# Optimization experiments

Hardware: AMD Instinct MI355X
Metric: run time of the kernel (lower is better)

The kernel has to match this reference:

```python
import jax, jax.numpy as jnp
import numpy as np

HEAD_DIM = 256
V_DIM = 256
HIDDEN = 1024
SCALE_BASE = 512
GAMMA = 0.96875
BATCH, SEQ = 4, 4096


def _dup_interleave(m):
    # (L, d/2) -> (L, d), duplicating each column consecutively
    return jnp.repeat(m, 2, axis=-1)


def _rotate_every_two(x):
    x1 = x[..., ::2]
    x2 = x[..., 1::2]
    return jnp.stack([-x2, x1], axis=-1).reshape(x.shape)


def _xpos(x, downscale=False):
    # x: (B, L, head_dim); offset=0 path of XPOS.forward
    B, L, Dh = x.shape
    half = Dh // 2
    scale_buf = (jnp.arange(0, Dh, 2, dtype=jnp.float32) + 0.4 * Dh) / (1.4 * Dh)  # (half,)
    pos = jnpp = jnp.arange(L, dtype=jnp.float32)
    scale = scale_buf[None, :] ** (pos / SCALE_BASE)[:, None]  # (L, half)
    inv_freq = 1.0 / (10000.0 ** (jnp.arange(half, dtype=jnp.float32) / half))
    sinusoid = pos[:, None] * inv_freq[None, :]  # (L, half)
    sin, cos = jnp.sin(sinusoid), jnp.cos(sinusoid)
    if downscale:
        scale = 1.0 / scale
    cos_s = _dup_interleave(cos * scale)  # (L, Dh)
    sin_s = _dup_interleave(sin * scale)
    return x * cos_s[None] + _rotate_every_two(x) * sin_s[None]


def _decay_matrix(L):
    n = jnp.arange(L)[:, None]
    m = jnp.arange(L)[None, :]
    mask = n >= m
    expo = jnp.where(mask, n - m, 0).astype(jnp.float32)
    return jnp.where(mask, GAMMA ** expo, 0.0)  # (L, L)


def setup_inputs() -> dict:
    key = jax.random.key(0)
    k1, k2, k3, k4 = jax.random.split(key, 4)
    X = jax.random.normal(k1, (BATCH, SEQ, HIDDEN), dtype=jnp.float32)
    W_Q = jax.random.normal(k2, (HIDDEN, HEAD_DIM), dtype=jnp.float32) / HIDDEN
    W_K = jax.random.normal(k3, (HIDDEN, HEAD_DIM), dtype=jnp.float32) / HIDDEN
    W_V = jax.random.normal(k4, (HIDDEN, V_DIM), dtype=jnp.float32) / HIDDEN
    return {"X": X, "W_Q": W_Q, "W_K": W_K, "W_V": W_V}


def reference(X, W_Q, W_K, W_V):
    L = X.shape[1]
    Q = _xpos(X @ W_Q)                      # (B, L, Dh)
    K = _xpos(X @ W_K, downscale=True)      # (B, L, Dh)
    V = X @ W_V                             # (B, L, Dv)
    D = _decay_matrix(L)                    # (L, L)
    ret = jnp.einsum('bqd,bkd->bqk', Q, K) * D[None]  # (B, L, L)
    return ret @ V                          # (B, L, Dv)
```

## Files before the change

### kernel.cpp

```cpp
#include <hip/hip_runtime.h>
#include <hip/hip_bf16.h>
#include <cstdint>
#include <cstddef>

#define L_SEQ 4096
#define BATCH_N 4
#define HID 1024
#define DH 256
#define LOG2_GAMMA (-0.045803689613124953f)

typedef __attribute__((ext_vector_type(8))) short short8;
typedef __attribute__((ext_vector_type(4))) float floatx4;

__device__ __forceinline__ unsigned short f2bf(float f) {
    union { float f; unsigned int u; } v; v.f = f;
    unsigned int r = (v.u + 0x7FFFu + ((v.u >> 16) & 1u)) >> 16;
    return (unsigned short)r;
}

__device__ __forceinline__ void async_copy16(const unsigned short* gsrc,
                                             unsigned short* lds) {
    __builtin_amdgcn_global_load_lds(
        (const __attribute__((address_space(1))) unsigned int*)gsrc,
        (__attribute__((address_space(3))) unsigned int*)lds, 16, 0, 0);
}

__global__ __launch_bounds__(256) void convert_x_kernel(
    const float* __restrict__ X, unsigned short* __restrict__ Xb)
{
    const int i = (blockIdx.x * 256 + threadIdx.x) * 4;
    const float4 v = *(const float4*)&X[i];
    ushort4 p;
    p.x = f2bf(v.x); p.y = f2bf(v.y); p.z = f2bf(v.z); p.w = f2bf(v.w);
    *(ushort4*)&Xb[i] = p;
}

__global__ __launch_bounds__(256) void transpose_w_kernel(
    const float* __restrict__ WQ, const float* __restrict__ WK,
    const float* __restrict__ WV, unsigned short* __restrict__ Wt)
{
    __shared__ float Ts[64][68];
    const int n0 = blockIdx.x * 64;
    const int k0 = blockIdx.y * 64;
    const int seg = n0 >> 8;
    const float* __restrict__ W = (seg == 0) ? WQ : (seg == 1) ? WK : WV;
    const int nl0 = n0 & 255;

    const int t  = threadIdx.x;
    const int r  = t >> 4;
    const int c4 = (t & 15) * 4;
    #pragma unroll
    for (int i = 0; i < 4; ++i) {
        const int kk = r + i * 16;
        const float4 v = *(const float4*)&W[(size_t)(k0 + kk) * DH + nl0 + c4];
        Ts[c4 + 0][kk] = v.x;
        Ts[c4 + 1][kk] = v.y;
        Ts[c4 + 2][kk] = v.z;
        Ts[c4 + 3][kk] = v.w;
    }
    __syncthreads();
    const int rn = t >> 3;
    const int c8 = (t & 7) * 8;
    #pragma unroll
    for (int i = 0; i < 2; ++i) {
        const int rr = rn + i * 32;
        ushort4 p0, p1;
        p0.x = f2bf(Ts[rr][c8 + 0]); p0.y = f2bf(Ts[rr][c8 + 1]);
        p0.z = f2bf(Ts[rr][c8 + 2]); p0.w = f2bf(Ts[rr][c8 + 3]);
        p1.x = f2bf(Ts[rr][c8 + 4]); p1.y = f2bf(Ts[rr][c8 + 5]);
        p1.z = f2bf(Ts[rr][c8 + 6]); p1.w = f2bf(Ts[rr][c8 + 7]);
        unsigned short* dst = &Wt[(size_t)(n0 + rr) * HID + k0 + c8];
        *(ushort4*)dst       = p0;
        *(ushort4*)(dst + 4) = p1;
    }
}

__global__ __launch_bounds__(256) void gemm_qkv_kernel(
    const unsigned short* __restrict__ Wt,
    const unsigned short* __restrict__ Xb,
    unsigned short* __restrict__ Qo,
    unsigned short* __restrict__ Ko,
    unsigned short* __restrict__ VtG)
{
    __shared__ unsigned short Wa[128][32];
    __shared__ unsigned short Xs[128][32];

    const int n0 = blockIdx.x * 128;
    const int p0 = blockIdx.y * 128;
    const int t    = threadIdx.x;
    const int w    = t >> 6;
    const int lane = t & 63;
    const int quad = lane >> 4;
    const int l16  = lane & 15;
    const int wn   = (w & 1) * 64;
    const int wp   = (w >> 1) * 64;

    const int srow = w * 32 + (lane >> 2);
    const int scol = (lane & 3) * 8;

    floatx4 acc[4][4];
    #pragma unroll
    for (int i = 0; i < 4; ++i)
        #pragma unroll
        for (int j = 0; j < 4; ++j) acc[i][j] = (floatx4){0.f, 0.f, 0.f, 0.f};

    for (int k0 = 0; k0 < HID; k0 += 32) {
        __syncthreads();
        #pragma unroll
        for (int is = 0; is < 2; ++is) {
            const unsigned short* ga =
                &Wt[(size_t)(n0 + srow + is * 16) * HID + k0 + scol];
            const unsigned short* gb =
                &Xb[(size_t)(p0 + srow + is * 16) * HID + k0 + scol];
            async_copy16(ga, &Wa[w * 32 + is * 16][0]);
            async_copy16(gb, &Xs[w * 32 + is * 16][0]);
        }
        __syncthreads();

        short8 af[4], bf[4];
        #pragma unroll
        for (int nt = 0; nt < 4; ++nt)
            af[nt] = *(const short8*)&Wa[wn + nt * 16 + l16][quad * 8];
        #pragma unroll
        for (int pt = 0; pt < 4; ++pt)
            bf[pt] = *(const short8*)&Xs[wp + pt * 16 + l16][quad * 8];
        #pragma unroll
        for (int nt = 0; nt < 4; ++nt)
            #pragma unroll
            for (int pt = 0; pt < 4; ++pt)
                acc[nt][pt] = __builtin_amdgcn_mfma_f32_16x16x32_bf16(
                    af[nt], bf[pt], acc[nt][pt], 0, 0, 0);
    }

    const int seg = n0 >> 8;
    #pragma unroll
    for (int nt = 0; nt < 4; ++nt) {
        const int nfeat = n0 + wn + nt * 16 + quad * 4;
        const int d0 = nfeat & 255;
        #pragma unroll
        for (int pt = 0; pt < 4; ++pt) {
            const int pg  = p0 + wp + pt * 16 + l16;
            const int b   = pg >> 12;
            const int pos = pg & (L_SEQ - 1);
            if (seg == 2) {
                #pragma unroll
                for (int g = 0; g < 4; ++g)
                    VtG[(((size_t)(b * 256 + d0 + g)) << 12) + pos] =
                        f2bf(acc[nt][pt][g]);
            } else {
                const float e = (float)pos * (1.0f / 512.0f);
                float res[4];
                #pragma unroll
                for (int h = 0; h < 4; h += 2) {
                    const int d  = d0 + h;
                    const int i2 = d >> 1;
                    const float sb = ((float)d + 102.4f) * (1.0f / 358.4f);
                    float sc = exp2f(log2f(sb) * e);
                    if (seg == 1) sc = 1.0f / sc;
                    const float invf = exp2f(-13.287712379549449f *
                                             ((float)i2 * (1.0f / 128.0f)));
                    float s, c;
                    sincosf((float)pos * invf, &s, &c);
                    const float cs = c * sc, ss = s * sc;
                    const float xe = acc[nt][pt][h], xo = acc[nt][pt][h + 1];
                    res[h]     = xe * cs - xo * ss;
                    res[h + 1] = xo * cs + xe * ss;
                }
                ushort4 pk;
                pk.x = f2bf(res[0]); pk.y = f2bf(res[1]);
                pk.z = f2bf(res[2]); pk.w = f2bf(res[3]);
                unsigned short* orow =
                    ((seg == 0) ? Qo : Ko) + (size_t)pg * DH + d0;
                *(ushort4*)orow = pk;
            }
        }
    }
}

__global__ __launch_bounds__(256) void retention_kernel(
    const unsigned short* __restrict__ Q,
    const unsigned short* __restrict__ K,
    const unsigned short* __restrict__ VtG,
    float* __restrict__ O)
{
    __shared__ short Qs[64][264];
    __shared__ short Ks[32][264];
    __shared__ short Vt[256][40];
    __shared__ short Ss[64][40];

    const int qt = blockIdx.x;
    const int b  = blockIdx.y;
    const int t  = threadIdx.x;
    const int q0 = qt * 64;

    const int w    = t >> 6;
    const int lane = t & 63;
    const int quad = lane >> 4;
    const int l16  = lane & 15;
    const int w16  = w * 16;

    const size_t rbase = (size_t)b * L_SEQ * DH;
    const size_t vbase = ((size_t)b * DH) << 12;

    {
        const unsigned short* src = Q + rbase + (size_t)q0 * DH;
        #pragma unroll
        for (int i = 0; i < 8; ++i) {
            const int row = i * 8 + (t >> 5);
            const int col = (t & 31) * 8;
            *(uint4*)&Qs[row][col] = *(const uint4*)&src[row * DH + col];
        }
    }

    floatx4 o[16];
    #pragma unroll
    for (int f = 0; f < 16; ++f) o[f] = (floatx4){0.f, 0.f, 0.f, 0.f};

    int kstart = q0 - 512;
    if (kstart < 0) kstart = 0;

    for (int k0 = kstart; k0 < q0 + 64; k0 += 32) {
        __syncthreads();
        {
            const unsigned short* src = K + rbase + (size_t)k0 * DH;
            #pragma unroll
            for (int i = 0; i < 4; ++i) {
                const int row = i * 8 + (t >> 5);
                const int col = (t & 31) * 8;
                *(uint4*)&Ks[row][col] = *(const uint4*)&src[row * DH + col];
            }
        }
        {
            const int koff = (t & 7) * 4;
            #pragma unroll
            for (int i = 0; i < 8; ++i) {
                const int c = (t >> 3) + 32 * i;
                *(uint2*)&Vt[c][koff] =
                    *(const uint2*)&VtG[vbase + ((size_t)c << 12) + k0 + koff];
            }
        }
        __syncthreads();

        #pragma unroll
        for (int ntile = 0; ntile < 2; ++ntile) {
            floatx4 s = (floatx4){0.f, 0.f, 0.f, 0.f};
            #pragma unroll
            for (int d8 = 0; d8 < 8; ++d8) {
                const short8 a   = *(const short8*)&Qs[w16 + l16][d8 * 32 + quad * 8];
                const short8 bfr = *(const short8*)&Ks[ntile * 16 + l16][d8 * 32 + quad * 8];
                s = __builtin_amdgcn_mfma_f32_16x16x32_bf16(a, bfr, s, 0, 0, 0);
            }
            const int kpos = k0 + ntile * 16 + l16;
            #pragma unroll
            for (int g = 0; g < 4; ++g) {
                const int qpos = q0 + w16 + quad * 4 + g;
                const int d = qpos - kpos;
                const float p = (d >= 0) ? s[g] * exp2f((float)d * LOG2_GAMMA) : 0.0f;
                Ss[w16 + quad * 4 + g][ntile * 16 + l16] = (short)f2bf(p);
            }
        }
        __syncthreads();

        {
            const short8 a = *(const short8*)&Ss[w16 + l16][quad * 8];
            #pragma unroll
            for (int f = 0; f < 16; ++f) {
                const short8 bfr = *(const short8*)&Vt[f * 16 + l16][quad * 8];
                o[f] = __builtin_amdgcn_mfma_f32_16x16x32_bf16(a, bfr, o[f], 0, 0, 0);
            }
        }
    }

    #pragma unroll
    for (int f = 0; f < 16; ++f) {
        #pragma unroll
        for (int g = 0; g < 4; ++g) {
            const int qpos = q0 + w16 + quad * 4 + g;
            O[rbase + (size_t)qpos * DH + f * 16 + l16] = o[f][g];
        }
    }
}

extern "C" void kernel_launch(void* const* d_in, const int* in_sizes, int n_in,
                              void* d_out, int out_size, void* d_ws, size_t ws_size,
                              hipStream_t stream)
{
    const float* X  = (const float*)d_in[0];
    const float* WQ = (const float*)d_in[1];
    const float* WK = (const float*)d_in[2];
    const float* WV = (const float*)d_in[3];
    float* out = (float*)d_out;

    const size_t per = (size_t)BATCH_N * L_SEQ * DH;
    unsigned short* Qw  = (unsigned short*)d_ws;
    unsigned short* Kw  = Qw + per;
    unsigned short* Vtw = Kw + per;
    unsigned short* Xbw = Vtw + per;
    unsigned short* Wtw = Xbw + (size_t)16384 * HID;

    convert_x_kernel<<<16384, 256, 0, stream>>>(X, Xbw);
    transpose_w_kernel<<<dim3(12, 16), 256, 0, stream>>>(WQ, WK, WV, Wtw);

    gemm_qkv_kernel<<<dim3(6, 128), 256, 0, stream>>>(Wtw, Xbw, Qw, Kw, Vtw);

    retention_kernel<<<dim3(L_SEQ / 64, BATCH_N), 256, 0, stream>>>(Qw, Kw, Vtw, out);
}
```

Baseline: 190.6 us.

## Prefetch K/V into registers, widen key tile, keep Q in registers, remap GEMM blocks

The retention kernel now holds each warp's Q fragments in registers instead of LDS. It processes 64 keys per iteration instead of 32 and prefetches the next K/V tile into registers while computing the current one. Score tiles are kept per warp in LDS, which removes one block barrier per iteration. The QKV GEMM uses a 1D grid with an XCD-aware block remap so blocks sharing X rows land on the same XCD for L2 reuse. The costs are higher register pressure (Q fragments plus prefetch buffers plus accumulators), which may reduce occupancy, and one redundant prefetch of the first tile on the final iteration.

Result: slower. 260.1 us (+36.5%).

```diff
diff --git a/kernel.cpp b/kernel.cpp
--- a/kernel.cpp
+++ b/kernel.cpp
@@ -24,6 +24,7 @@
         (const __attribute__((address_space(1))) unsigned int*)gsrc,
         (__attribute__((address_space(3))) unsigned int*)lds, 16, 0, 0);
 }
+
 
 __global__ __launch_bounds__(256) void convert_x_kernel(
     const float* __restrict__ X, unsigned short* __restrict__ Xb)
@@ -85,8 +86,12 @@
     __shared__ unsigned short Wa[128][32];
     __shared__ unsigned short Xs[128][32];
 
-    const int n0 = blockIdx.x * 128;
-    const int p0 = blockIdx.y * 128;
+    const int idx = blockIdx.x;
+    const int xcd = idx & 7;
+    const int j   = idx >> 3;
+    const int n0  = (j % 6) * 128;
+    const int p0  = (xcd * 16 + (j / 6)) * 128;
+
     const int t    = threadIdx.x;
     const int w    = t >> 6;
     const int lane = t & 63;
@@ -102,7 +107,7 @@
     #pragma unroll
     for (int i = 0; i < 4; ++i)
         #pragma unroll
-        for (int j = 0; j < 4; ++j) acc[i][j] = (floatx4){0.f, 0.f, 0.f, 0.f};
+        for (int jj = 0; jj < 4; ++jj) acc[i][jj] = (floatx4){0.f, 0.f, 0.f, 0.f};
 
     for (int k0 = 0; k0 < HID; k0 += 32) {
         __syncthreads();
@@ -117,19 +122,19 @@
         }
         __syncthreads();
 
-        short8 af[4], bf[4];
+        short8 af[4], bfv[4];
         #pragma unroll
         for (int nt = 0; nt < 4; ++nt)
             af[nt] = *(const short8*)&Wa[wn + nt * 16 + l16][quad * 8];
         #pragma unroll
         for (int pt = 0; pt < 4; ++pt)
-            bf[pt] = *(const short8*)&Xs[wp + pt * 16 + l16][quad * 8];
+            bfv[pt] = *(const short8*)&Xs[wp + pt * 16 + l16][quad * 8];
         #pragma unroll
         for (int nt = 0; nt < 4; ++nt)
             #pragma unroll
             for (int pt = 0; pt < 4; ++pt)
                 acc[nt][pt] = __builtin_amdgcn_mfma_f32_16x16x32_bf16(
-                    af[nt], bf[pt], acc[nt][pt], 0, 0, 0);
+                    af[nt], bfv[pt], acc[nt][pt], 0, 0, 0);
     }
 
     const int seg = n0 >> 8;
@@ -159,8 +164,9 @@
                     if (seg == 1) sc = 1.0f / sc;
                     const float invf = exp2f(-13.287712379549449f *
                                              ((float)i2 * (1.0f / 128.0f)));
+                    const float th = (float)pos * invf;
                     float s, c;
-                    sincosf((float)pos * invf, &s, &c);
+                    sincosf(th, &s, &c);
                     const float cs = c * sc, ss = s * sc;
                     const float xe = acc[nt][pt][h], xo = acc[nt][pt][h + 1];
                     res[h]     = xe * cs - xo * ss;
@@ -183,10 +189,9 @@
     const unsigned short* __restrict__ VtG,
     float* __restrict__ O)
 {
-    __shared__ short Qs[64][264];
-    __shared__ short Ks[32][264];
-    __shared__ short Vt[256][40];
-    __shared__ short Ss[64][40];
+    __shared__ short Ks[64][264];
+    __shared__ short Vt[256][72];
+    __shared__ short Ss[4][16][72];
 
     const int qt = blockIdx.x;
     const int b  = blockIdx.y;
@@ -202,14 +207,18 @@
     const size_t rbase = (size_t)b * L_SEQ * DH;
     const size_t vbase = ((size_t)b * DH) << 12;
 
+    const int krow = t >> 5;
+    const int kcol = (t & 31) * 8;
+    const int vc   = t >> 3;
+    const int vk   = (t & 7) * 8;
+
+    short8 qf[8];
     {
-        const unsigned short* src = Q + rbase + (size_t)q0 * DH;
-        #pragma unroll
-        for (int i = 0; i < 8; ++i) {
-            const int row = i * 8 + (t >> 5);
-            const int col = (t & 31) * 8;
-            *(uint4*)&Qs[row][col] = *(const uint4*)&src[row * DH + col];
-        }
+        const unsigned short* qrow =
+            Q + rbase + (size_t)(q0 + w16 + l16) * DH + quad * 8;
+        #pragma unroll
+        for (int d8 = 0; d8 < 8; ++d8)
+            qf[d8] = *(const short8*)(qrow + d8 * 32);
     }
 
     floatx4 o[16];
@@ -219,54 +228,61 @@
     int kstart = q0 - 512;
     if (kstart < 0) kstart = 0;
 
-    for (int k0 = kstart; k0 < q0 + 64; k0 += 32) {
+    uint4 kreg[8], vreg[8];
+    #pragma unroll
+    for (int i = 0; i < 8; ++i) {
+        kreg[i] = *(const uint4*)&K[rbase + (size_t)(kstart + i * 8 + krow) * DH + kcol];
+        vreg[i] = *(const uint4*)&VtG[vbase + ((size_t)(vc + i * 32) << 12) + kstart + vk];
+    }
+
+    for (int k0 = kstart; k0 < q0 + 64; k0 += 64) {
         __syncthreads();
+        #pragma unroll
+        for (int i = 0; i < 8; ++i) {
+            *(uint4*)&Ks[i * 8 + krow][kcol] = kreg[i];
+            *(uint4*)&Vt[vc + i * 32][vk]    = vreg[i];
+        }
         {
-            const unsigned short* src = K + rbase + (size_t)k0 * DH;
-            #pragma unroll
-            for (int i = 0; i < 4; ++i) {
-                const int row = i * 8 + (t >> 5);
-                const int col = (t & 31) * 8;
-                *(uint4*)&Ks[row][col] = *(const uint4*)&src[row * DH + col];
-            }
-        }
-        {
-            const int koff = (t & 7) * 4;
+            const int kn = (k0 + 64 < q0 + 64) ? (k0 + 64) : kstart;
             #pragma unroll
             for (int i = 0; i < 8; ++i) {
-                const int c = (t >> 3) + 32 * i;
-                *(uint2*)&Vt[c][koff] =
-                    *(const uint2*)&VtG[vbase + ((size_t)c << 12) + k0 + koff];
+                kreg[i] = *(const uint4*)&K[rbase + (size_t)(kn + i * 8 + krow) * DH + kcol];
+                vreg[i] = *(const uint4*)&VtG[vbase + ((size_t)(vc + i * 32) << 12) + kn + vk];
             }
         }
         __syncthreads();
 
         #pragma unroll
-        for (int ntile = 0; ntile < 2; ++ntile) {
+        for (int nt = 0; nt < 4; ++nt) {
             floatx4 s = (floatx4){0.f, 0.f, 0.f, 0.f};
             #pragma unroll
             for (int d8 = 0; d8 < 8; ++d8) {
-                const short8 a   = *(const short8*)&Qs[w16 + l16][d8 * 32 + quad * 8];
-                const short8 bfr = *(const short8*)&Ks[ntile * 16 + l16][d8 * 32 + quad * 8];
-                s = __builtin_amdgcn_mfma_f32_16x16x32_bf16(a, bfr, s, 0, 0, 0);
-            }
-            const int kpos = k0 + ntile * 16 + l16;
+                const short8 bfr =
+                    *(const short8*)&Ks[nt * 16 + l16][d8 * 32 + quad * 8];
+                s = __builtin_amdgcn_mfma_f32_16x16x32_bf16(qf[d8], bfr, s, 0, 0, 0);
+            }
+            const int kpos = k0 + nt * 16 + l16;
             #pragma unroll
             for (int g = 0; g < 4; ++g) {
                 const int qpos = q0 + w16 + quad * 4 + g;
                 const int d = qpos - kpos;
                 const float p = (d >= 0) ? s[g] * exp2f((float)d * LOG2_GAMMA) : 0.0f;
-                Ss[w16 + quad * 4 + g][ntile * 16 + l16] = (short)f2bf(p);
-            }
-        }
-        __syncthreads();
+                Ss[w][quad * 4 + g][nt * 16 + l16] = (short)f2bf(p);
+            }
+        }
 
         {
-            const short8 a = *(const short8*)&Ss[w16 + l16][quad * 8];
+            const short8 a0 = *(const short8*)&Ss[w][l16][quad * 8];
+            const short8 a1 = *(const short8*)&Ss[w][l16][32 + quad * 8];
             #pragma unroll
             for (int f = 0; f < 16; ++f) {
-                const short8 bfr = *(const short8*)&Vt[f * 16 + l16][quad * 8];
-                o[f] = __builtin_amdgcn_mfma_f32_16x16x32_bf16(a, bfr, o[f], 0, 0, 0);
+                const short8 b0 = *(const short8*)&Vt[f * 16 + l16][quad * 8];
+                o[f] = __builtin_amdgcn_mfma_f32_16x16x32_bf16(a0, b0, o[f], 0, 0, 0);
+            }
+            #pragma unroll
+            for (int f = 0; f < 16; ++f) {
+                const short8 b1 = *(const short8*)&Vt[f * 16 + l16][32 + quad * 8];
+                o[f] = __builtin_amdgcn_mfma_f32_16x16x32_bf16(a1, b1, o[f], 0, 0, 0);
             }
         }
     }
@@ -301,7 +317,7 @@
     convert_x_kernel<<<16384, 256, 0, stream>>>(X, Xbw);
     transpose_w_kernel<<<dim3(12, 16), 256, 0, stream>>>(WQ, WK, WV, Wtw);
 
-    gemm_qkv_kernel<<<dim3(6, 128), 256, 0, stream>>>(Wtw, Xbw, Qw, Kw, Vtw);
-
-    retention_kernel<<<dim3(L_SEQ / 64, BATCH_N), 256, 0, stream>>>(Qw, Kw, Vtw, out);
-}
+    gemm_qkv_kernel<<<768, 256, 0, stream>>>(Wtw, Xbw, Qw, Kw, Vtw);
+
+    retention_kernel<<<dim3(64, BATCH_N), 256, 0, stream>>>(Qw, Kw, Vtw, out);
+}
```
